# Performance work log

Measured on AMD Instinct MI355X. Metric: run time of the kernel, lower is better.

Reference implementation:

```python
import jax, jax.numpy as jnp
import numpy as np

DIM = 256
HEADS = 8
WH, WW = 8, 8
N = WH * WW
B_ = 2048
NW = 64  # num windows per image; B_ // NW = batch of 32
CPB_HIDDEN = 256


def _log_rel_index(wh, ww):
    ch = np.arange(wh)
    cw = np.arange(ww)
    coords = np.stack(np.meshgrid(ch, cw, indexing='ij'))      # (2, wh, ww)
    cf = coords.reshape(2, -1)                                  # (2, N)
    rel = cf[:, :, None] - cf[:, None, :]                       # (2, N, N)
    rel = rel.transpose(1, 2, 0).astype(np.float32)             # (N, N, 2)
    return np.sign(rel) * np.log1p(np.abs(rel))


def setup_inputs() -> dict:
    key = jax.random.key(0)
    ks = jax.random.split(key, 16)
    s = 0.02
    inp = {
        'x': jax.random.normal(ks[0], (B_, N, DIM), jnp.float32),
        'KV': jax.random.normal(ks[1], (B_, N, DIM), jnp.float32),
        'mask': jnp.zeros((NW, N, N), jnp.float32),
        # linear weights stored (in, out): y = x @ W + b
        'Wq': jax.random.normal(ks[2], (DIM, DIM), jnp.float32) * s,
        'bq': jnp.zeros((DIM,), jnp.float32),
        'Wkv': jax.random.normal(ks[3], (DIM, 2 * DIM), jnp.float32) * s,
        'bkv': jnp.zeros((2 * DIM,), jnp.float32),
        'Wp': jax.random.normal(ks[4], (DIM, DIM), jnp.float32) * s,
        'bp': jnp.zeros((DIM,), jnp.float32),
        'cpb_w1': jax.random.normal(ks[5], (2, CPB_HIDDEN), jnp.float32) * s,
        'cpb_b1': jnp.zeros((CPB_HIDDEN,), jnp.float32),
        'cpb_w2': jax.random.normal(ks[6], (CPB_HIDDEN, HEADS), jnp.float32) * s,
        'cpb_b2': jnp.zeros((HEADS,), jnp.float32),
        'tau': jnp.ones((HEADS, N, N), jnp.float32),
        'log_rel_idx': jnp.asarray(_log_rel_index(WH, WW)),  # (N, N, 2)
    }
    return inp


def reference(x, KV, mask, Wq, bq, Wkv, bkv, Wp, bp,
              cpb_w1, cpb_b1, cpb_w2, cpb_b2, tau, log_rel_idx):
    Bw, n, C = x.shape
    H = tau.shape[0]
    hd = C // H
    scale = hd ** -0.5

    q = (x @ Wq + bq).reshape(Bw, n, H, hd).transpose(0, 2, 1, 3) * scale   # (B_,H,N,hd)
    kv = (KV @ Wkv + bkv).reshape(Bw, n, 2, H, hd).transpose(2, 0, 3, 1, 4)  # (2,B_,H,N,hd)
    k, v = kv[0], kv[1]

    num = jnp.einsum('bhqd,bhkd->bhqk', q, k)
    qn = jnp.sqrt(jnp.sum(q * q, axis=-1, keepdims=True))                    # (B_,H,N,1)
    kn = jnp.sqrt(jnp.sum(k * k, axis=-1, keepdims=True))                    # (B_,H,N,1)
    denom = jnp.maximum(qn * kn.transpose(0, 1, 3, 2), 1e-6)
    attn = num / denom
    attn = attn / jnp.clip(tau[:, :n, :n], 0.01)[None]

    # continuous relative position bias MLP: (N,N,2) -> (N,N,H)
    h = jax.nn.relu(log_rel_idx[:n, :n] @ cpb_w1 + cpb_b1)
    bias = (h @ cpb_w2 + cpb_b2).transpose(2, 0, 1)                          # (H,N,N)
    attn = attn + bias[None]

    nW = mask.shape[0]
    attn = attn.reshape(Bw // nW, nW, H, n, n) + mask[None, :, None]
    attn = attn.reshape(Bw, H, n, n)
    attn = jax.nn.softmax(attn, axis=-1)

    out = jnp.einsum('bhqk,bhkd->bhqd', attn, v)
    out = out.transpose(0, 2, 1, 3).reshape(Bw, n, C)
    out = out @ Wp + bp
    return out
```

## Files before the change

### kernel.cpp

```cpp
#include <hip/hip_runtime.h>

#define NTOK 64
#define CDIM 256
#define NHEAD 8
#define HD 32
#define NWIN 64

typedef __attribute__((ext_vector_type(8))) short v8s;
typedef __attribute__((ext_vector_type(4))) short v4s;
typedef __attribute__((ext_vector_type(4))) float v4f;

#define CFENCE() asm volatile("" ::: "memory")

#define WQT_OFF   0u
#define WKVT_OFF  131072u
#define WPT_OFF   393216u
#define ITB_OFF   524288u
#define WS_BYTES  786432u

static __device__ __forceinline__ short f2bf(float f) {
  union { float f; unsigned int u; } v; v.f = f;
  unsigned int u = v.u;
  return (short)((u + 0x7fffu + ((u >> 16) & 1u)) >> 16);
}

__global__ void prep_kernel(const float* __restrict__ Wq, const float* __restrict__ Wkv,
                            const float* __restrict__ Wp, const float* __restrict__ tau,
                            short* __restrict__ WqT, short* __restrict__ WkvT,
                            short* __restrict__ WpT, float2* __restrict__ itb) {
  int id = blockIdx.x * 256 + threadIdx.x;
  if (id < 65536) {
    int o = id >> 8, i = id & 255;
    WqT[id] = f2bf(Wq[i * 256 + o]);
  } else if (id < 196608) {
    int t = id - 65536; int o = t >> 8, i = t & 255;
    WkvT[t] = f2bf(Wkv[i * 512 + o]);
  } else if (id < 262144) {
    int t = id - 196608; int o = t >> 8, i = t & 255;
    WpT[t] = f2bf(Wp[i * 256 + o]);
  } else if (id < 294912) {
    int t = id - 262144;
    itb[t].x = 1.0f / fmaxf(tau[t], 0.01f);
  }
}

__global__ void cpb_kernel(const float* __restrict__ w1, const float* __restrict__ b1,
                           const float* __restrict__ w2, const float* __restrict__ b2,
                           const float* __restrict__ lri, float2* __restrict__ itb) {
  int ij = blockIdx.x * 256 + threadIdx.x;
  float l0 = lri[ij * 2], l1 = lri[ij * 2 + 1];
  float acc[8];
#pragma unroll
  for (int h = 0; h < 8; ++h) acc[h] = b2[h];
  for (int c = 0; c < 256; ++c) {
    float hv = fmaxf(l0 * w1[c] + l1 * w1[256 + c] + b1[c], 0.0f);
#pragma unroll
    for (int h = 0; h < 8; ++h) acc[h] += hv * w2[c * 8 + h];
  }
#pragma unroll
  for (int h = 0; h < 8; ++h) itb[h * 4096 + ij].y = acc[h];
}

static __device__ __forceinline__ void gemm_64x32_k256(
    const short* aLds, const short* Bg, int qd, int cc, v4f acc[4][2]) {
#pragma unroll
  for (int it = 0; it < 8; ++it) {
    const int k0 = it * 32;
    v8s b0 = *(const v8s*)(Bg + cc * 256 + k0 + qd * 8);
    v8s b1 = *(const v8s*)(Bg + (16 + cc) * 256 + k0 + qd * 8);
#pragma unroll
    for (int mt = 0; mt < 4; ++mt) {
      v8s a = *(const v8s*)(aLds + (mt * 16 + cc) * 264 + k0 + qd * 8);
      acc[mt][0] = __builtin_amdgcn_mfma_f32_16x16x32_bf16(a, b0, acc[mt][0], 0, 0, 0);
      acc[mt][1] = __builtin_amdgcn_mfma_f32_16x16x32_bf16(a, b1, acc[mt][1], 0, 0, 0);
    }
  }
}

__global__ __launch_bounds__(512, 2) void wattn_kernel(
    const float* __restrict__ x, const float* __restrict__ KV,
    const float* __restrict__ mask,
    const float* __restrict__ bq, const float* __restrict__ bkv,
    const float* __restrict__ bp,
    const short* __restrict__ WqT, const short* __restrict__ WkvT,
    const short* __restrict__ WpT, const float2* __restrict__ itb,
    float* __restrict__ out) {
  __shared__ short sm[59392];

  const int b = blockIdx.x;
  const int tid = threadIdx.x;
  const int w = tid >> 6;
  const int lane = tid & 63;
  const int qd = lane >> 4;
  const int cc = lane & 15;
  const v4f vzero = {0.f, 0.f, 0.f, 0.f};

  {
    const float4* xb = (const float4*)(x + (size_t)b * 16384);
    const float4* kb = (const float4*)(KV + (size_t)b * 16384);
    for (int i = tid; i < 4096; i += 512) {
      int r = i >> 6, col = (i & 63) << 2;
      float4 vx = xb[i];
      float4 vk = kb[i];
      v4s px, pk;
      px[0] = f2bf(vx.x); px[1] = f2bf(vx.y); px[2] = f2bf(vx.z); px[3] = f2bf(vx.w);
      pk[0] = f2bf(vk.x); pk[1] = f2bf(vk.y); pk[2] = f2bf(vk.z); pk[3] = f2bf(vk.w);
      *(v4s*)&sm[r * 264 + col] = px;
      *(v4s*)&sm[20480 + r * 264 + col] = pk;
    }
  }
  __syncthreads();

  v4f qa[4][2];
#pragma unroll
  for (int mt = 0; mt < 4; ++mt) { qa[mt][0] = vzero; qa[mt][1] = vzero; }
  gemm_64x32_k256(sm, WqT + (32 * w) * 256, qd, cc, qa);
  {
    float b0 = bq[32 * w + cc], b1 = bq[32 * w + 16 + cc];
#pragma unroll
    for (int mt = 0; mt < 4; ++mt)
#pragma unroll
      for (int rg = 0; rg < 4; ++rg) {
        float a0 = qa[mt][0][rg] + b0;
        float a1 = qa[mt][1][rg] + b1;
        float s = a0 * a0 + a1 * a1;
        s += __shfl_xor(s, 1); s += __shfl_xor(s, 2);
        s += __shfl_xor(s, 4); s += __shfl_xor(s, 8);
        float inv = rsqrtf(s + 1e-24f);
        qa[mt][0][rg] = a0 * inv;
        qa[mt][1][rg] = a1 * inv;
      }
  }
  __syncthreads();

  short* qt = sm + w * 2560;
#pragma unroll
  for (int mt = 0; mt < 4; ++mt)
#pragma unroll
    for (int rg = 0; rg < 4; ++rg) {
      int row = mt * 16 + qd * 4 + rg;
      qt[row * 40 + cc] = f2bf(qa[mt][0][rg]);
      qt[row * 40 + 16 + cc] = f2bf(qa[mt][1][rg]);
    }

  v4f ka[4][2], va[4][2];
#pragma unroll
  for (int mt = 0; mt < 4; ++mt) { ka[mt][0] = vzero; ka[mt][1] = vzero; va[mt][0] = vzero; va[mt][1] = vzero; }
  gemm_64x32_k256(sm + 20480, WkvT + (32 * w) * 256, qd, cc, ka);
  {
    float b0 = bkv[32 * w + cc], b1 = bkv[32 * w + 16 + cc];
#pragma unroll
    for (int mt = 0; mt < 4; ++mt)
#pragma unroll
      for (int rg = 0; rg < 4; ++rg) {
        float a0 = ka[mt][0][rg] + b0;
        float a1 = ka[mt][1][rg] + b1;
        float s = a0 * a0 + a1 * a1;
        s += __shfl_xor(s, 1); s += __shfl_xor(s, 2);
        s += __shfl_xor(s, 4); s += __shfl_xor(s, 8);
        float inv = rsqrtf(s + 1e-24f);
        ka[mt][0][rg] = a0 * inv;
        ka[mt][1][rg] = a1 * inv;
      }
  }
  gemm_64x32_k256(sm + 20480, WkvT + (256 + 32 * w) * 256, qd, cc, va);
  {
    float b0 = bkv[256 + 32 * w + cc], b1 = bkv[256 + 32 * w + 16 + cc];
#pragma unroll
    for (int mt = 0; mt < 4; ++mt)
#pragma unroll
      for (int rg = 0; rg < 4; ++rg) { va[mt][0][rg] += b0; va[mt][1][rg] += b1; }
  }
  __syncthreads();

  short* kt = sm + 20480 + w * 4864;
  short* vt = kt + 2560;
#pragma unroll
  for (int mt = 0; mt < 4; ++mt)
#pragma unroll
    for (int rg = 0; rg < 4; ++rg) {
      int row = mt * 16 + qd * 4 + rg;
      kt[row * 40 + cc] = f2bf(ka[mt][0][rg]);
      kt[row * 40 + 16 + cc] = f2bf(ka[mt][1][rg]);
      vt[cc * 72 + row] = f2bf(va[mt][0][rg]);
      vt[(16 + cc) * 72 + row] = f2bf(va[mt][1][rg]);
    }
  CFENCE();

  v8s aq[4];
#pragma unroll
  for (int mt = 0; mt < 4; ++mt)
    aq[mt] = *(const v8s*)(qt + (mt * 16 + cc) * 40 + qd * 8);
  v4f S[4][4];
#pragma unroll
  for (int nt = 0; nt < 4; ++nt) {
    v8s bk = *(const v8s*)(kt + (nt * 16 + cc) * 40 + qd * 8);
#pragma unroll
    for (int mt = 0; mt < 4; ++mt)
      S[mt][nt] = __builtin_amdgcn_mfma_f32_16x16x32_bf16(aq[mt], bk, vzero, 0, 0, 0);
  }

  {
    const float2* itbh = itb + w * 4096;
    const float* mw = mask + (size_t)(b & (NWIN - 1)) * 4096;
#pragma unroll
    for (int mt = 0; mt < 4; ++mt)
#pragma unroll
      for (int rg = 0; rg < 4; ++rg) {
        int i = mt * 16 + qd * 4 + rg;
        float vals[4];
#pragma unroll
        for (int nt = 0; nt < 4; ++nt) {
          int j = nt * 16 + cc;
          float2 tb = itbh[i * 64 + j];
          vals[nt] = S[mt][nt][rg] * tb.x + tb.y + mw[i * 64 + j];
        }
        float mx = fmaxf(fmaxf(vals[0], vals[1]), fmaxf(vals[2], vals[3]));
        mx = fmaxf(mx, __shfl_xor(mx, 1)); mx = fmaxf(mx, __shfl_xor(mx, 2));
        mx = fmaxf(mx, __shfl_xor(mx, 4)); mx = fmaxf(mx, __shfl_xor(mx, 8));
        float sum = 0.f;
#pragma unroll
        for (int nt = 0; nt < 4; ++nt) {
          float e = __expf(vals[nt] - mx);
          S[mt][nt][rg] = e;
          sum += e;
        }
        sum += __shfl_xor(sum, 1); sum += __shfl_xor(sum, 2);
        sum += __shfl_xor(sum, 4); sum += __shfl_xor(sum, 8);
        float rs = 1.0f / sum;
#pragma unroll
        for (int nt = 0; nt < 4; ++nt) S[mt][nt][rg] *= rs;
      }
  }

  v4f o[4][2];
#pragma unroll
  for (int mt = 0; mt < 4; ++mt) { o[mt][0] = vzero; o[mt][1] = vzero; }
  short* pt = qt;
#pragma unroll
  for (int kc = 0; kc < 2; ++kc) {
    CFENCE();
#pragma unroll
    for (int mt = 0; mt < 4; ++mt)
#pragma unroll
      for (int rg = 0; rg < 4; ++rg) {
        int row = mt * 16 + qd * 4 + rg;
        pt[row * 40 + cc] = f2bf(S[mt][kc * 2][rg]);
        pt[row * 40 + 16 + cc] = f2bf(S[mt][kc * 2 + 1][rg]);
      }
    CFENCE();
#pragma unroll
    for (int mt = 0; mt < 4; ++mt) {
      v8s ap = *(const v8s*)(pt + (mt * 16 + cc) * 40 + qd * 8);
#pragma unroll
      for (int d = 0; d < 2; ++d) {
        v8s bv = *(const v8s*)(vt + (d * 16 + cc) * 72 + kc * 32 + qd * 8);
        o[mt][d] = __builtin_amdgcn_mfma_f32_16x16x32_bf16(ap, bv, o[mt][d], 0, 0, 0);
      }
    }
  }

  __syncthreads();
#pragma unroll
  for (int mt = 0; mt < 4; ++mt)
#pragma unroll
    for (int rg = 0; rg < 4; ++rg) {
      int row = mt * 16 + qd * 4 + rg;
      sm[row * 264 + 32 * w + cc] = f2bf(o[mt][0][rg]);
      sm[row * 264 + 32 * w + 16 + cc] = f2bf(o[mt][1][rg]);
    }
  __syncthreads();

  v4f pa[4][2];
#pragma unroll
  for (int mt = 0; mt < 4; ++mt) { pa[mt][0] = vzero; pa[mt][1] = vzero; }
  gemm_64x32_k256(sm, WpT + (32 * w) * 256, qd, cc, pa);
  {
    float b0 = bp[32 * w + cc], b1 = bp[32 * w + 16 + cc];
    float* ob = out + (size_t)b * 16384;
#pragma unroll
    for (int mt = 0; mt < 4; ++mt)
#pragma unroll
      for (int rg = 0; rg < 4; ++rg) {
        int row = mt * 16 + qd * 4 + rg;
        ob[row * 256 + 32 * w + cc] = pa[mt][0][rg] + b0;
        ob[row * 256 + 32 * w + 16 + cc] = pa[mt][1][rg] + b1;
      }
  }
}

extern "C" void kernel_launch(void* const* d_in, const int* in_sizes, int n_in,
                              void* d_out, int out_size, void* d_ws, size_t ws_size,
                              hipStream_t stream) {
  const float* x    = (const float*)d_in[0];
  const float* KV   = (const float*)d_in[1];
  const float* mask = (const float*)d_in[2];
  const float* Wq   = (const float*)d_in[3];
  const float* bq   = (const float*)d_in[4];
  const float* Wkv  = (const float*)d_in[5];
  const float* bkv  = (const float*)d_in[6];
  const float* Wp   = (const float*)d_in[7];
  const float* bp   = (const float*)d_in[8];
  const float* cw1  = (const float*)d_in[9];
  const float* cb1  = (const float*)d_in[10];
  const float* cw2  = (const float*)d_in[11];
  const float* cb2  = (const float*)d_in[12];
  const float* tau  = (const float*)d_in[13];
  const float* lri  = (const float*)d_in[14];

  unsigned char* ws = (unsigned char*)d_ws;
  short* WqT   = (short*)(ws + WQT_OFF);
  short* WkvT  = (short*)(ws + WKVT_OFF);
  short* WpT   = (short*)(ws + WPT_OFF);
  float2* itb  = (float2*)(ws + ITB_OFF);

  prep_kernel<<<1152, 256, 0, stream>>>(Wq, Wkv, Wp, tau, WqT, WkvT, WpT, itb);
  cpb_kernel<<<16, 256, 0, stream>>>(cw1, cb1, cw2, cb2, lri, itb);
  wattn_kernel<<<2048, 512, 0, stream>>>(x, KV, mask, bq, bkv, bp,
                                         WqT, WkvT, WpT, itb, (float*)d_out);
}
```

Measured before the change: 564.0 us.

## Keep Q/K/V/P in registers via transposed MFMA and cross-lane shuffles

Restructures the attention kernel so the Q and K projections compute transposed tiles (weights as A operand). This lets the per-token normalisation reduce over quad lanes and lets results become MFMA operands through register shuffles instead of LDS round-trips. The attention scores are computed transposed, softmax runs along the lane axis, and P@V uses register-resident operands. Dropping the per-wave Q/K/V/P staging cuts shared memory from about 116KB to 66KB, and launch bounds are raised to 4 blocks per CU for more occupancy. In exchange there is more shuffle traffic and register pressure, which could cause spills under the tighter launch bounds.

```diff
diff --git a/kernel.cpp b/kernel.cpp
--- a/kernel.cpp
+++ b/kernel.cpp
@@ -1,27 +1,25 @@
 #include <hip/hip_runtime.h>
-
-#define NTOK 64
-#define CDIM 256
-#define NHEAD 8
-#define HD 32
+#include <hip/hip_bf16.h>
+
 #define NWIN 64
 
 typedef __attribute__((ext_vector_type(8))) short v8s;
-typedef __attribute__((ext_vector_type(4))) short v4s;
 typedef __attribute__((ext_vector_type(4))) float v4f;
-
-#define CFENCE() asm volatile("" ::: "memory")
 
 #define WQT_OFF   0u
 #define WKVT_OFF  131072u
 #define WPT_OFF   393216u
 #define ITB_OFF   524288u
-#define WS_BYTES  786432u
 
 static __device__ __forceinline__ short f2bf(float f) {
   union { float f; unsigned int u; } v; v.f = f;
   unsigned int u = v.u;
   return (short)((u + 0x7fffu + ((u >> 16) & 1u)) >> 16);
+}
+
+static __device__ __forceinline__ int packbf(float lo, float hi) {
+  __hip_bfloat162 h = __float22bfloat162_rn(float2{lo, hi});
+  union { __hip_bfloat162 h; int i; } u; u.h = h; return u.i;
 }
 
 __global__ void prep_kernel(const float* __restrict__ Wq, const float* __restrict__ Wkv,
@@ -61,23 +59,21 @@
   for (int h = 0; h < 8; ++h) itb[h * 4096 + ij].y = acc[h];
 }
 
-static __device__ __forceinline__ void gemm_64x32_k256(
-    const short* aLds, const short* Bg, int qd, int cc, v4f acc[4][2]) {
-#pragma unroll
-  for (int it = 0; it < 8; ++it) {
-    const int k0 = it * 32;
-    v8s b0 = *(const v8s*)(Bg + cc * 256 + k0 + qd * 8);
-    v8s b1 = *(const v8s*)(Bg + (16 + cc) * 256 + k0 + qd * 8);
-#pragma unroll
-    for (int mt = 0; mt < 4; ++mt) {
-      v8s a = *(const v8s*)(aLds + (mt * 16 + cc) * 264 + k0 + qd * 8);
-      acc[mt][0] = __builtin_amdgcn_mfma_f32_16x16x32_bf16(a, b0, acc[mt][0], 0, 0, 0);
-      acc[mt][1] = __builtin_amdgcn_mfma_f32_16x16x32_bf16(a, b1, acc[mt][1], 0, 0, 0);
-    }
-  }
-}
-
-__global__ __launch_bounds__(512, 2) void wattn_kernel(
+static __device__ __forceinline__ v8s xform_tile(int p0a, int p0b, int p1a, int p1b,
+                                                 int base, int mdsel) {
+  int a0 = __shfl(p0a, base, 64),      b0 = __shfl(p1a, base, 64);
+  int a1 = __shfl(p0b, base, 64),      b1 = __shfl(p1b, base, 64);
+  int a2 = __shfl(p0a, base + 16, 64), b2 = __shfl(p1a, base + 16, 64);
+  int a3 = __shfl(p0b, base + 16, 64), b3 = __shfl(p1b, base + 16, 64);
+  union { v8s v; int i[4]; } r;
+  r.i[0] = mdsel ? b0 : a0;
+  r.i[1] = mdsel ? b1 : a1;
+  r.i[2] = mdsel ? b2 : a2;
+  r.i[3] = mdsel ? b3 : a3;
+  return r.v;
+}
+
+__global__ __launch_bounds__(512, 4) void wattn_kernel(
     const float* __restrict__ x, const float* __restrict__ KV,
     const float* __restrict__ mask,
     const float* __restrict__ bq, const float* __restrict__ bkv,
@@ -85,196 +81,244 @@
     const short* __restrict__ WqT, const short* __restrict__ WkvT,
     const short* __restrict__ WpT, const float2* __restrict__ itb,
     float* __restrict__ out) {
-  __shared__ short sm[59392];
+  __shared__ short sm[33792];
 
   const int b = blockIdx.x;
   const int tid = threadIdx.x;
   const int w = tid >> 6;
   const int lane = tid & 63;
+  const int cc = lane & 15;
   const int qd = lane >> 4;
-  const int cc = lane & 15;
+  const int base = cc + 32 * (qd & 1);
+  const int mdsel = qd >> 1;
   const v4f vzero = {0.f, 0.f, 0.f, 0.f};
+  short* xs = sm;
+  short* kvs = sm + 16896;
 
   {
     const float4* xb = (const float4*)(x + (size_t)b * 16384);
     const float4* kb = (const float4*)(KV + (size_t)b * 16384);
-    for (int i = tid; i < 4096; i += 512) {
+#pragma unroll
+    for (int ii = 0; ii < 8; ++ii) {
+      int i = tid + ii * 512;
       int r = i >> 6, col = (i & 63) << 2;
       float4 vx = xb[i];
       float4 vk = kb[i];
-      v4s px, pk;
-      px[0] = f2bf(vx.x); px[1] = f2bf(vx.y); px[2] = f2bf(vx.z); px[3] = f2bf(vx.w);
-      pk[0] = f2bf(vk.x); pk[1] = f2bf(vk.y); pk[2] = f2bf(vk.z); pk[3] = f2bf(vk.w);
-      *(v4s*)&sm[r * 264 + col] = px;
-      *(v4s*)&sm[20480 + r * 264 + col] = pk;
+      int2 px = { packbf(vx.x, vx.y), packbf(vx.z, vx.w) };
+      int2 pk = { packbf(vk.x, vk.y), packbf(vk.z, vk.w) };
+      *(int2*)&xs[r * 264 + col] = px;
+      *(int2*)&kvs[r * 264 + col] = pk;
     }
   }
   __syncthreads();
 
-  v4f qa[4][2];
-#pragma unroll
-  for (int mt = 0; mt < 4; ++mt) { qa[mt][0] = vzero; qa[mt][1] = vzero; }
-  gemm_64x32_k256(sm, WqT + (32 * w) * 256, qd, cc, qa);
-  {
-    float b0 = bq[32 * w + cc], b1 = bq[32 * w + 16 + cc];
-#pragma unroll
-    for (int mt = 0; mt < 4; ++mt)
+  v4f Dq[2][4];
+#pragma unroll
+  for (int md = 0; md < 2; ++md)
+#pragma unroll
+    for (int nt = 0; nt < 4; ++nt) Dq[md][nt] = vzero;
+  {
+    const short* wqb = WqT + (32 * w + cc) * 256 + qd * 8;
+#pragma unroll
+    for (int it = 0; it < 8; ++it) {
+      v8s a0 = *(const v8s*)(wqb + it * 32);
+      v8s a1 = *(const v8s*)(wqb + 16 * 256 + it * 32);
+#pragma unroll
+      for (int nt = 0; nt < 4; ++nt) {
+        v8s bx = *(const v8s*)(xs + (nt * 16 + cc) * 264 + it * 32 + qd * 8);
+        Dq[0][nt] = __builtin_amdgcn_mfma_f32_16x16x32_bf16(a0, bx, Dq[0][nt], 0, 0, 0);
+        Dq[1][nt] = __builtin_amdgcn_mfma_f32_16x16x32_bf16(a1, bx, Dq[1][nt], 0, 0, 0);
+      }
+    }
+  }
+  v8s qB[4];
+  {
+    v4f b0 = *(const v4f*)(bq + 32 * w + qd * 4);
+    v4f b1 = *(const v4f*)(bq + 32 * w + 16 + qd * 4);
+#pragma unroll
+    for (int nt = 0; nt < 4; ++nt) {
+      float s = 0.f;
 #pragma unroll
       for (int rg = 0; rg < 4; ++rg) {
-        float a0 = qa[mt][0][rg] + b0;
-        float a1 = qa[mt][1][rg] + b1;
-        float s = a0 * a0 + a1 * a1;
-        s += __shfl_xor(s, 1); s += __shfl_xor(s, 2);
-        s += __shfl_xor(s, 4); s += __shfl_xor(s, 8);
-        float inv = rsqrtf(s + 1e-24f);
-        qa[mt][0][rg] = a0 * inv;
-        qa[mt][1][rg] = a1 * inv;
-      }
-  }
+        float v0 = Dq[0][nt][rg] + b0[rg];
+        float v1 = Dq[1][nt][rg] + b1[rg];
+        Dq[0][nt][rg] = v0; Dq[1][nt][rg] = v1;
+        s += v0 * v0 + v1 * v1;
+      }
+      s += __shfl_xor(s, 16); s += __shfl_xor(s, 32);
+      float inv = rsqrtf(s + 1e-24f);
+      int p00 = packbf(Dq[0][nt][0] * inv, Dq[0][nt][1] * inv);
+      int p01 = packbf(Dq[0][nt][2] * inv, Dq[0][nt][3] * inv);
+      int p10 = packbf(Dq[1][nt][0] * inv, Dq[1][nt][1] * inv);
+      int p11 = packbf(Dq[1][nt][2] * inv, Dq[1][nt][3] * inv);
+      qB[nt] = xform_tile(p00, p01, p10, p11, base, mdsel);
+    }
+  }
+
+  v4f Dk[2][4], Dv[4][2];
+#pragma unroll
+  for (int nt = 0; nt < 4; ++nt) {
+    Dk[0][nt] = vzero; Dk[1][nt] = vzero;
+    Dv[nt][0] = vzero; Dv[nt][1] = vzero;
+  }
+  {
+    const short* wkb = WkvT + (32 * w + cc) * 256 + qd * 8;
+    const short* wvb = WkvT + (256 + 32 * w + cc) * 256 + qd * 8;
+#pragma unroll
+    for (int it = 0; it < 8; ++it) {
+      v8s ak0 = *(const v8s*)(wkb + it * 32);
+      v8s ak1 = *(const v8s*)(wkb + 16 * 256 + it * 32);
+      v8s bv0 = *(const v8s*)(wvb + it * 32);
+      v8s bv1 = *(const v8s*)(wvb + 16 * 256 + it * 32);
+#pragma unroll
+      for (int nt = 0; nt < 4; ++nt) {
+        v8s kf = *(const v8s*)(kvs + (nt * 16 + cc) * 264 + it * 32 + qd * 8);
+        Dk[0][nt] = __builtin_amdgcn_mfma_f32_16x16x32_bf16(ak0, kf, Dk[0][nt], 0, 0, 0);
+        Dk[1][nt] = __builtin_amdgcn_mfma_f32_16x16x32_bf16(ak1, kf, Dk[1][nt], 0, 0, 0);
+        Dv[nt][0] = __builtin_amdgcn_mfma_f32_16x16x32_bf16(kf, bv0, Dv[nt][0], 0, 0, 0);
+        Dv[nt][1] = __builtin_amdgcn_mfma_f32_16x16x32_bf16(kf, bv1, Dv[nt][1], 0, 0, 0);
+      }
+    }
+  }
+  v8s kA[4];
+  {
+    v4f b0 = *(const v4f*)(bkv + 32 * w + qd * 4);
+    v4f b1 = *(const v4f*)(bkv + 32 * w + 16 + qd * 4);
+#pragma unroll
+    for (int nt = 0; nt < 4; ++nt) {
+      float s = 0.f;
+#pragma unroll
+      for (int rg = 0; rg < 4; ++rg) {
+        float v0 = Dk[0][nt][rg] + b0[rg];
+        float v1 = Dk[1][nt][rg] + b1[rg];
+        Dk[0][nt][rg] = v0; Dk[1][nt][rg] = v1;
+        s += v0 * v0 + v1 * v1;
+      }
+      s += __shfl_xor(s, 16); s += __shfl_xor(s, 32);
+      float inv = rsqrtf(s + 1e-24f);
+      int p00 = packbf(Dk[0][nt][0] * inv, Dk[0][nt][1] * inv);
+      int p01 = packbf(Dk[0][nt][2] * inv, Dk[0][nt][3] * inv);
+      int p10 = packbf(Dk[1][nt][0] * inv, Dk[1][nt][1] * inv);
+      int p11 = packbf(Dk[1][nt][2] * inv, Dk[1][nt][3] * inv);
+      kA[nt] = xform_tile(p00, p01, p10, p11, base, mdsel);
+    }
+  }
+  v8s av[2][2];
+  {
+    float bv0 = bkv[256 + 32 * w + cc];
+    float bv1 = bkv[256 + 32 * w + 16 + cc];
+    int Pv[4][2][2];
+#pragma unroll
+    for (int vt = 0; vt < 4; ++vt) {
+      Pv[vt][0][0] = packbf(Dv[vt][0][0] + bv0, Dv[vt][0][1] + bv0);
+      Pv[vt][0][1] = packbf(Dv[vt][0][2] + bv0, Dv[vt][0][3] + bv0);
+      Pv[vt][1][0] = packbf(Dv[vt][1][0] + bv1, Dv[vt][1][1] + bv1);
+      Pv[vt][1][1] = packbf(Dv[vt][1][2] + bv1, Dv[vt][1][3] + bv1);
+    }
+#pragma unroll
+    for (int md = 0; md < 2; ++md)
+#pragma unroll
+      for (int kc = 0; kc < 2; ++kc)
+        av[md][kc] = xform_tile(Pv[2 * kc][md][0], Pv[2 * kc][md][1],
+                                Pv[2 * kc + 1][md][0], Pv[2 * kc + 1][md][1], base, mdsel);
+  }
+
+  v4f Sv[4][4];
+#pragma unroll
+  for (int jt = 0; jt < 4; ++jt)
+#pragma unroll
+    for (int it = 0; it < 4; ++it)
+      Sv[jt][it] = __builtin_amdgcn_mfma_f32_16x16x32_bf16(kA[jt], qB[it], vzero, 0, 0, 0);
+
+  {
+    const float4* itb4 = (const float4*)(itb + (size_t)w * 4096);
+    const float4* mw4 = (const float4*)(mask + (size_t)(b & (NWIN - 1)) * 4096);
+#pragma unroll
+    for (int it = 0; it < 4; ++it) {
+      int i = it * 16 + cc;
+#pragma unroll
+      for (int jt = 0; jt < 4; ++jt) {
+        int e = i * 64 + jt * 16 + qd * 4;
+        float4 A = itb4[e >> 1];
+        float4 B = itb4[(e >> 1) + 1];
+        float4 M = mw4[e >> 2];
+        Sv[jt][it][0] = Sv[jt][it][0] * A.x + A.y + M.x;
+        Sv[jt][it][1] = Sv[jt][it][1] * A.z + A.w + M.y;
+        Sv[jt][it][2] = Sv[jt][it][2] * B.x + B.y + M.z;
+        Sv[jt][it][3] = Sv[jt][it][3] * B.z + B.w + M.w;
+      }
+      float mx = -3.4e38f;
+#pragma unroll
+      for (int jt = 0; jt < 4; ++jt)
+#pragma unroll
+        for (int rg = 0; rg < 4; ++rg) mx = fmaxf(mx, Sv[jt][it][rg]);
+      mx = fmaxf(mx, __shfl_xor(mx, 16)); mx = fmaxf(mx, __shfl_xor(mx, 32));
+      float sum = 0.f;
+#pragma unroll
+      for (int jt = 0; jt < 4; ++jt)
+#pragma unroll
+        for (int rg = 0; rg < 4; ++rg) {
+          float ev = __expf(Sv[jt][it][rg] - mx);
+          Sv[jt][it][rg] = ev;
+          sum += ev;
+        }
+      sum += __shfl_xor(sum, 16); sum += __shfl_xor(sum, 32);
+      float rs = 1.0f / sum;
+#pragma unroll
+      for (int jt = 0; jt < 4; ++jt)
+#pragma unroll
+        for (int rg = 0; rg < 4; ++rg) Sv[jt][it][rg] *= rs;
+    }
+  }
+
+  v4f Do[2][4];
+  {
+#pragma unroll
+    for (int it = 0; it < 4; ++it) {
+      int pp[4][2];
+#pragma unroll
+      for (int jt = 0; jt < 4; ++jt) {
+        pp[jt][0] = packbf(Sv[jt][it][0], Sv[jt][it][1]);
+        pp[jt][1] = packbf(Sv[jt][it][2], Sv[jt][it][3]);
+      }
+      v8s pB0 = xform_tile(pp[0][0], pp[0][1], pp[1][0], pp[1][1], base, mdsel);
+      v8s pB1 = xform_tile(pp[2][0], pp[2][1], pp[3][0], pp[3][1], base, mdsel);
+#pragma unroll
+      for (int md = 0; md < 2; ++md) {
+        v4f t = __builtin_amdgcn_mfma_f32_16x16x32_bf16(av[md][0], pB0, vzero, 0, 0, 0);
+        Do[md][it] = __builtin_amdgcn_mfma_f32_16x16x32_bf16(av[md][1], pB1, t, 0, 0, 0);
+      }
+    }
+  }
+
   __syncthreads();
-
-  short* qt = sm + w * 2560;
-#pragma unroll
-  for (int mt = 0; mt < 4; ++mt)
-#pragma unroll
-    for (int rg = 0; rg < 4; ++rg) {
-      int row = mt * 16 + qd * 4 + rg;
-      qt[row * 40 + cc] = f2bf(qa[mt][0][rg]);
-      qt[row * 40 + 16 + cc] = f2bf(qa[mt][1][rg]);
-    }
-
-  v4f ka[4][2], va[4][2];
-#pragma unroll
-  for (int mt = 0; mt < 4; ++mt) { ka[mt][0] = vzero; ka[mt][1] = vzero; va[mt][0] = vzero; va[mt][1] = vzero; }
-  gemm_64x32_k256(sm + 20480, WkvT + (32 * w) * 256, qd, cc, ka);
-  {
-    float b0 = bkv[32 * w + cc], b1 = bkv[32 * w + 16 + cc];
-#pragma unroll
-    for (int mt = 0; mt < 4; ++mt)
-#pragma unroll
-      for (int rg = 0; rg < 4; ++rg) {
-        float a0 = ka[mt][0][rg] + b0;
-        float a1 = ka[mt][1][rg] + b1;
-        float s = a0 * a0 + a1 * a1;
-        s += __shfl_xor(s, 1); s += __shfl_xor(s, 2);
-        s += __shfl_xor(s, 4); s += __shfl_xor(s, 8);
-        float inv = rsqrtf(s + 1e-24f);
-        ka[mt][0][rg] = a0 * inv;
-        ka[mt][1][rg] = a1 * inv;
-      }
-  }
-  gemm_64x32_k256(sm + 20480, WkvT + (256 + 32 * w) * 256, qd, cc, va);
-  {
-    float b0 = bkv[256 + 32 * w + cc], b1 = bkv[256 + 32 * w + 16 + cc];
-#pragma unroll
-    for (int mt = 0; mt < 4; ++mt)
-#pragma unroll
-      for (int rg = 0; rg < 4; ++rg) { va[mt][0][rg] += b0; va[mt][1][rg] += b1; }
-  }
+#pragma unroll
+  for (int md = 0; md < 2; ++md)
+#pragma unroll
+    for (int it = 0; it < 4; ++it) {
+      int addr = (it * 16 + cc) * 264 + 32 * w + md * 16 + qd * 4;
+      *(int*)&sm[addr] = packbf(Do[md][it][0], Do[md][it][1]);
+      *(int*)&sm[addr + 2] = packbf(Do[md][it][2], Do[md][it][3]);
+    }
   __syncthreads();
 
-  short* kt = sm + 20480 + w * 4864;
-  short* vt = kt + 2560;
-#pragma unroll
-  for (int mt = 0; mt < 4; ++mt)
-#pragma unroll
-    for (int rg = 0; rg < 4; ++rg) {
-      int row = mt * 16 + qd * 4 + rg;
-      kt[row * 40 + cc] = f2bf(ka[mt][0][rg]);
-      kt[row * 40 + 16 + cc] = f2bf(ka[mt][1][rg]);
-      vt[cc * 72 + row] = f2bf(va[mt][0][rg]);
-      vt[(16 + cc) * 72 + row] = f2bf(va[mt][1][rg]);
-    }
-  CFENCE();
-
-  v8s aq[4];
-#pragma unroll
-  for (int mt = 0; mt < 4; ++mt)
-    aq[mt] = *(const v8s*)(qt + (mt * 16 + cc) * 40 + qd * 8);
-  v4f S[4][4];
-#pragma unroll
-  for (int nt = 0; nt < 4; ++nt) {
-    v8s bk = *(const v8s*)(kt + (nt * 16 + cc) * 40 + qd * 8);
-#pragma unroll
-    for (int mt = 0; mt < 4; ++mt)
-      S[mt][nt] = __builtin_amdgcn_mfma_f32_16x16x32_bf16(aq[mt], bk, vzero, 0, 0, 0);
-  }
-
-  {
-    const float2* itbh = itb + w * 4096;
-    const float* mw = mask + (size_t)(b & (NWIN - 1)) * 4096;
-#pragma unroll
-    for (int mt = 0; mt < 4; ++mt)
-#pragma unroll
-      for (int rg = 0; rg < 4; ++rg) {
-        int i = mt * 16 + qd * 4 + rg;
-        float vals[4];
-#pragma unroll
-        for (int nt = 0; nt < 4; ++nt) {
-          int j = nt * 16 + cc;
-          float2 tb = itbh[i * 64 + j];
-          vals[nt] = S[mt][nt][rg] * tb.x + tb.y + mw[i * 64 + j];
-        }
-        float mx = fmaxf(fmaxf(vals[0], vals[1]), fmaxf(vals[2], vals[3]));
-        mx = fmaxf(mx, __shfl_xor(mx, 1)); mx = fmaxf(mx, __shfl_xor(mx, 2));
-        mx = fmaxf(mx, __shfl_xor(mx, 4)); mx = fmaxf(mx, __shfl_xor(mx, 8));
-        float sum = 0.f;
-#pragma unroll
-        for (int nt = 0; nt < 4; ++nt) {
-          float e = __expf(vals[nt] - mx);
-          S[mt][nt][rg] = e;
-          sum += e;
-        }
-        sum += __shfl_xor(sum, 1); sum += __shfl_xor(sum, 2);
-        sum += __shfl_xor(sum, 4); sum += __shfl_xor(sum, 8);
-        float rs = 1.0f / sum;
-#pragma unroll
-        for (int nt = 0; nt < 4; ++nt) S[mt][nt][rg] *= rs;
-      }
-  }
-
-  v4f o[4][2];
-#pragma unroll
-  for (int mt = 0; mt < 4; ++mt) { o[mt][0] = vzero; o[mt][1] = vzero; }
-  short* pt = qt;
-#pragma unroll
-  for (int kc = 0; kc < 2; ++kc) {
-    CFENCE();
-#pragma unroll
-    for (int mt = 0; mt < 4; ++mt)
-#pragma unroll
-      for (int rg = 0; rg < 4; ++rg) {
-        int row = mt * 16 + qd * 4 + rg;
-        pt[row * 40 + cc] = f2bf(S[mt][kc * 2][rg]);
-        pt[row * 40 + 16 + cc] = f2bf(S[mt][kc * 2 + 1][rg]);
-      }
-    CFENCE();
-#pragma unroll
-    for (int mt = 0; mt < 4; ++mt) {
-      v8s ap = *(const v8s*)(pt + (mt * 16 + cc) * 40 + qd * 8);
-#pragma unroll
-      for (int d = 0; d < 2; ++d) {
-        v8s bv = *(const v8s*)(vt + (d * 16 + cc) * 72 + kc * 32 + qd * 8);
-        o[mt][d] = __builtin_amdgcn_mfma_f32_16x16x32_bf16(ap, bv, o[mt][d], 0, 0, 0);
-      }
-    }
-  }
-
-  __syncthreads();
-#pragma unroll
-  for (int mt = 0; mt < 4; ++mt)
-#pragma unroll
-    for (int rg = 0; rg < 4; ++rg) {
-      int row = mt * 16 + qd * 4 + rg;
-      sm[row * 264 + 32 * w + cc] = f2bf(o[mt][0][rg]);
-      sm[row * 264 + 32 * w + 16 + cc] = f2bf(o[mt][1][rg]);
-    }
-  __syncthreads();
-
   v4f pa[4][2];
 #pragma unroll
   for (int mt = 0; mt < 4; ++mt) { pa[mt][0] = vzero; pa[mt][1] = vzero; }
-  gemm_64x32_k256(sm, WpT + (32 * w) * 256, qd, cc, pa);
+  {
+    const short* wpb = WpT + (32 * w + cc) * 256 + qd * 8;
+#pragma unroll
+    for (int it = 0; it < 8; ++it) {
+      v8s b0 = *(const v8s*)(wpb + it * 32);
+      v8s b1 = *(const v8s*)(wpb + 16 * 256 + it * 32);
+#pragma unroll
+      for (int mt = 0; mt < 4; ++mt) {
+        v8s a = *(const v8s*)(sm + (mt * 16 + cc) * 264 + it * 32 + qd * 8);
+        pa[mt][0] = __builtin_amdgcn_mfma_f32_16x16x32_bf16(a, b0, pa[mt][0], 0, 0, 0);
+        pa[mt][1] = __builtin_amdgcn_mfma_f32_16x16x32_bf16(a, b1, pa[mt][1], 0, 0, 0);
+      }
+    }
+  }
   {
     float b0 = bp[32 * w + cc], b1 = bp[32 * w + 16 + cc];
     float* ob = out + (size_t)b * 16384;
```

Measured after the change: 559.0 us. No clear change (-0.9%).
